# Optimization experiments

Hardware: AMD Instinct MI355X
Metric: run time of the kernel (lower is better)

Reference implementation:

```python
import jax, jax.numpy as jnp
import numpy as np

D_MODEL = 1024
HEADS = 16
DEPTH = D_MODEL // HEADS
B, S = 4, 4096
EPS_K = 1e-6  # kernel feature epsilon
EPS_LN = 1e-6


def setup_inputs() -> dict:
    key = jax.random.key(0)
    ks = jax.random.split(key, 8)
    lecun = 1.0 / np.sqrt(D_MODEL)  # LecunNormal stddev
    glorot = np.sqrt(2.0 / (D_MODEL + D_MODEL))  # keras Dense default
    return {
        "q": jax.random.normal(ks[0], (B, S, D_MODEL), jnp.float32),
        "k": jax.random.normal(ks[1], (B, S, D_MODEL), jnp.float32),
        "v": jax.random.normal(ks[2], (B, S, D_MODEL), jnp.float32),
        "mask": jnp.ones((B, S), jnp.float32),
        "wq": jax.random.normal(ks[3], (D_MODEL, D_MODEL), jnp.float32) * lecun,
        "wk": jax.random.normal(ks[4], (D_MODEL, D_MODEL), jnp.float32) * lecun,
        "wv": jax.random.normal(ks[5], (D_MODEL, D_MODEL), jnp.float32) * lecun,
        "ln_gamma": jnp.ones((D_MODEL,), jnp.float32),
        "ln_beta": jnp.zeros((D_MODEL,), jnp.float32),
        "dense_w": jax.random.normal(ks[6], (D_MODEL, D_MODEL), jnp.float32) * glorot,
        "dense_b": jnp.zeros((D_MODEL,), jnp.float32),
    }


def _layernorm(x, g, b):
    m = jnp.mean(x, axis=-1, keepdims=True)
    var = jnp.var(x, axis=-1, keepdims=True)
    return (x - m) * jax.lax.rsqrt(var + EPS_LN) * g + b


def _split_heads(x):
    bsz, sl, _ = x.shape
    return x.reshape(bsz, sl, HEADS, DEPTH).transpose(0, 2, 1, 3)  # [B,H,S,depth]


def reference(q, k, v, mask, wq, wk, wv, ln_gamma, ln_beta, dense_w, dense_b):
    bsz = q.shape[0]
    em = mask[:, None, :, None]  # [B,1,S,1] broadcast over heads/depth
    qh = _split_heads(_layernorm(q @ wq, ln_gamma, ln_beta))
    kh = _split_heads(_layernorm(k @ wk, ln_gamma, ln_beta))
    vh = _split_heads(_layernorm(v @ wv, ln_gamma, ln_beta))
    q_prime = jax.nn.relu(qh) + EPS_K
    k_prime = (jax.nn.relu(kh) + EPS_K) * em
    vh = vh * em
    kv = jnp.einsum('bhnd,bhne->bhde', k_prime, vh)  # [B,H,depth,depth]
    z = 1.0 / (jnp.einsum('bhnd,bhd->bhn', q_prime, k_prime.sum(axis=-2)) + EPS_K)
    att = jnp.einsum('bhnd,bhde,bhn->bhne', q_prime, kv, z)  # [B,H,S,depth]
    # Faithful to original: reshape WITHOUT transposing heads back.
    att = att.reshape(bsz, -1, D_MODEL)  # [B,S,d_model]
    out = att @ dense_w + dense_b
    return _layernorm(out, ln_gamma, ln_beta)
```

## Files before the change

### kernel.cpp

```cpp
#include <hip/hip_runtime.h>
#include <hip/hip_bf16.h>
#include <stdint.h>

#define D_MODEL 1024
#define S_LEN   4096
#define BATCH   4
#define HEADS   16
#define DEPTH   64
#define ROWS    (BATCH*S_LEN)
#define EPS_K_F 1e-6f
#define EPS_LN_F 1e-6f

typedef __attribute__((ext_vector_type(8))) short short8;
typedef __attribute__((ext_vector_type(4))) float f32x4;

__device__ __forceinline__ unsigned short f2bf(float f) {
  union { float f; unsigned u; } x; x.f = f;
  unsigned r = x.u + 0x7FFF + ((x.u >> 16) & 1);
  return (unsigned short)(r >> 16);
}
__device__ __forceinline__ float bf2f(unsigned short b) {
  union { unsigned u; float f; } x; x.u = ((unsigned)b) << 16;
  return x.f;
}
__device__ __forceinline__ void gload16(const void* g, void* l) {
  __builtin_amdgcn_global_load_lds(
      (const __attribute__((address_space(1))) void*)g,
      (__attribute__((address_space(3))) void*)l, 16, 0, 0);
}

__global__ __launch_bounds__(256) void wtrans_k(
    const float* __restrict__ W, unsigned short* __restrict__ Wt,
    const float* __restrict__ qsrc, unsigned short* __restrict__ qdst,
    int slice) {
  __shared__ float tile[32][33];
  int n0 = blockIdx.x * 32, k0 = blockIdx.y * 32;
  int tx = threadIdx.x & 31, ty = threadIdx.x >> 5;
  #pragma unroll
  for (int i = 0; i < 32; i += 8)
    tile[ty + i][tx] = W[(size_t)(k0 + ty + i) * D_MODEL + n0 + tx];
  if (qsrc) {
    int bid = blockIdx.y * 32 + blockIdx.x;
    size_t base = (size_t)slice * 4194304 + (size_t)bid * 4096 +
                  (size_t)threadIdx.x * 8;
    #pragma unroll
    for (int it = 0; it < 2; ++it) {
      size_t off = base + (size_t)it * 2048;
      float4 a = *(const float4*)(qsrc + off);
      float4 b = *(const float4*)(qsrc + off + 4);
      uint4 pk;
      pk.x = (unsigned)f2bf(a.x) | ((unsigned)f2bf(a.y) << 16);
      pk.y = (unsigned)f2bf(a.z) | ((unsigned)f2bf(a.w) << 16);
      pk.z = (unsigned)f2bf(b.x) | ((unsigned)f2bf(b.y) << 16);
      pk.w = (unsigned)f2bf(b.z) | ((unsigned)f2bf(b.w) << 16);
      *(uint4*)(qdst + off) = pk;
    }
  }
  __syncthreads();
  #pragma unroll
  for (int i = 0; i < 32; i += 8)
    Wt[(size_t)(n0 + ty + i) * D_MODEL + k0 + tx] = f2bf(tile[tx][ty + i]);
}


#define GEMM_EPILOGUE(HASBIAS)                                               \
  if (HASBIAS) {                                                             \
    float bv[4];                                                             \
    _Pragma("unroll")                                                        \
    for (int n = 0; n < 4; ++n)                                              \
      bv[n] = bias[(int)n0 + wcn * 64 + n * 16 + l15];                       \
    _Pragma("unroll")                                                        \
    for (int m = 0; m < 8; ++m)                                              \
      _Pragma("unroll")                                                      \
      for (int n = 0; n < 4; ++n)                                            \
        _Pragma("unroll")                                                    \
        for (int j = 0; j < 4; ++j)                                          \
          acc[m][n][j] += bv[n];                                             \
  }                                                                          \
  int seg = (int)(n0 >> 6) + wcn;                                            \
  _Pragma("unroll")                                                          \
  for (int m = 0; m < 8; ++m) {                                              \
    float s[4], s2[4];                                                       \
    _Pragma("unroll")                                                        \
    for (int j = 0; j < 4; ++j) {                                            \
      float a = 0.f, b = 0.f;                                                \
      _Pragma("unroll")                                                      \
      for (int n = 0; n < 4; ++n) { float x = acc[m][n][j]; a += x; b += x*x; } \
      s[j] = a; s2[j] = b;                                                   \
    }                                                                        \
    _Pragma("unroll")                                                        \
    for (int off = 1; off < 16; off <<= 1) {                                 \
      _Pragma("unroll")                                                      \
      for (int j = 0; j < 4; ++j) {                                          \
        s[j]  += __shfl_xor(s[j],  off);                                     \
        s2[j] += __shfl_xor(s2[j], off);                                     \
      }                                                                      \
    }                                                                        \
    if (l15 == 0) {                                                          \
      _Pragma("unroll")                                                      \
      for (int j = 0; j < 4; ++j) {                                          \
        int rg = (int)m0 + wr * 128 + m * 16 + lhi * 4 + j;                  \
        psum[rg * 16 + seg] = s[j];                                          \
        psq [rg * 16 + seg] = s2[j];                                         \
      }                                                                      \
    }                                                                        \
  }                                                                          \
  _Pragma("unroll")                                                          \
  for (int m = 0; m < 8; ++m)                                                \
    _Pragma("unroll")                                                        \
    for (int j = 0; j < 4; ++j) {                                            \
      size_t row = m0 + wr * 128 + m * 16 + lhi * 4 + j;                     \
      _Pragma("unroll")                                                      \
      for (int n = 0; n < 4; ++n) {                                          \
        int col = (int)n0 + wcn * 64 + n * 16 + l15;                         \
        Cb[row * N + col] = f2bf(acc[m][n][j]);                              \
      }                                                                      \
    }

#define STAGE_HALF(kof_, slot_, h_) do {                                     \
    _Pragma("unroll")                                                        \
    for (int j = 0; j < 2; ++j) {                                            \
      int idx = j * 512 + t; int r_ = idx >> 2; int cs_ = idx & 3;           \
      int c_ = cs_ ^ ((r_ >> 1) & 3);                                        \
      gload16(A + (m0 + r_) * (size_t)K + (kof_) + (h_) * 32 + c_ * 8,       \
              &Al[slot_][(h_) * 8192 + idx * 8]);                            \
    }                                                                        \
    _Pragma("unroll")                                                        \
    for (int j = 0; j < 2; ++j) {                                            \
      int idx = j * 512 + t; int r_ = idx >> 2; int cs_ = idx & 3;           \
      int c_ = cs_ ^ ((r_ >> 1) & 3);                                        \
      gload16(Bt + (n0 + r_) * (size_t)K + (kof_) + (h_) * 32 + c_ * 8,      \
              &Bl[slot_][(h_) * 8192 + idx * 8]);                            \
    }                                                                        \
  } while (0)

#define PH_READ_B(kk_)                                                       \
    _Pragma("unroll")                                                        \
    for (int n = 0; n < 4; ++n) {                                            \
      int rb_ = wcn * 64 + n * 16 + l15;                                     \
      bfr[n] = *(const short8*)&Bl[slot][(kk_) * 8192 + rb_ * 32 + cswz];    \
    }
#define PH_READ_A(kk_, mh_)                                                  \
    _Pragma("unroll")                                                        \
    for (int m = 0; m < 4; ++m) {                                            \
      int ra_ = wr * 128 + ((mh_) * 4 + m) * 16 + l15;                       \
      af[m] = *(const short8*)&Al[slot][(kk_) * 8192 + ra_ * 32 + cswz];     \
    }
#define PH_MFMA(mh_)                                                         \
    __builtin_amdgcn_s_setprio(1);                                           \
    _Pragma("unroll")                                                        \
    for (int m = 0; m < 4; ++m)                                              \
      _Pragma("unroll")                                                      \
      for (int n = 0; n < 4; ++n)                                            \
        acc[(mh_) * 4 + m][n] = __builtin_amdgcn_mfma_f32_16x16x32_bf16(     \
            af[m], bfr[n], acc[(mh_) * 4 + m][n], 0, 0, 0);                  \
    __builtin_amdgcn_s_setprio(0);
#define LGKM0                                                                \
    asm volatile("s_waitcnt lgkmcnt(0)" ::: "memory");                       \
    __builtin_amdgcn_sched_barrier(0);

#define SIDE_PACK_STORE(chunk_) do {                                         \
    uint4 pk_;                                                               \
    pk_.x = (unsigned)f2bf(sreg0.x) | ((unsigned)f2bf(sreg0.y) << 16);       \
    pk_.y = (unsigned)f2bf(sreg0.z) | ((unsigned)f2bf(sreg0.w) << 16);       \
    pk_.z = (unsigned)f2bf(sreg1.x) | ((unsigned)f2bf(sreg1.y) << 16);       \
    pk_.w = (unsigned)f2bf(sreg1.z) | ((unsigned)f2bf(sreg1.w) << 16);       \
    *(uint4*)(side_dst + sbase + (size_t)(chunk_) * 4096) = pk_;             \
  } while (0)
#define SIDE_LOAD(chunk_) do {                                               \
    const float* sp_ = side_src + sbase + (size_t)(chunk_) * 4096;           \
    sreg0 = *(const float4*)sp_; sreg1 = *(const float4*)(sp_ + 4);          \
  } while (0)

#define TAIL_TILE(slot_) do {                                                \
    const int slot = (slot_);                                                \
    short8 af[4], bfr[4];                                                    \
    PH_READ_B(0) PH_READ_A(0, 0) LGKM0 PH_MFMA(0)                            \
    PH_READ_A(0, 1) LGKM0 PH_MFMA(1)                                         \
    PH_READ_B(1) PH_READ_A(1, 0) LGKM0 PH_MFMA(0)                            \
    PH_READ_A(1, 1) LGKM0 PH_MFMA(1)                                         \
  } while (0)

template <bool SIDECAR>
__global__ __launch_bounds__(512) void gemm_bt_k(
    const unsigned short* __restrict__ A,
    const unsigned short* __restrict__ Bt,
    unsigned short* __restrict__ Cb,
    float* __restrict__ psum, float* __restrict__ psq,
    const float* __restrict__ bias,
    const float* __restrict__ side_src,
    unsigned short* __restrict__ side_dst,
    int M, int N, int K) {
  __shared__ unsigned short Al[2][16384];
  __shared__ unsigned short Bl[2][16384];
  int t = threadIdx.x;
  int lane = t & 63, wid = t >> 6;
  int wr = wid >> 2, wcn = wid & 3;
  int l15 = lane & 15, lhi = lane >> 4;
  const int cswz = (lhi ^ ((l15 >> 1) & 3)) << 3;
  int p = blockIdx.x;
  int cb = (p >> 3) & 3;
  int rb = (p & 7) | ((p >> 5) << 3);
  size_t m0 = (size_t)rb * 256, n0 = (size_t)cb * 256;
  f32x4 acc[8][4] = {};

  const int KT = K >> 6;

  float4 sreg0 = {}, sreg1 = {};
  size_t sbase = (size_t)p * 65536 + (size_t)t * 8;

  if (SIDECAR) SIDE_LOAD(0);
  STAGE_HALF(0, 0, 0);  STAGE_HALF(0, 0, 1);
  STAGE_HALF(64, 1, 0); STAGE_HALF(64, 1, 1);
  asm volatile("s_waitcnt vmcnt(8)" ::: "memory");
  __builtin_amdgcn_s_barrier();
  __builtin_amdgcn_sched_barrier(0);

  for (int kt = 0; kt < KT - 2; ++kt) {
    const int slot = kt & 1;
    short8 af[4], bfr[4];
    PH_READ_B(0)
    PH_READ_A(0, 0)
    LGKM0
    PH_MFMA(0)
    PH_READ_A(0, 1)
    LGKM0
    __builtin_amdgcn_s_barrier();
    __builtin_amdgcn_sched_barrier(0);
    STAGE_HALF((kt + 2) << 6, slot, 0);
    __builtin_amdgcn_sched_barrier(0);
    PH_MFMA(1)
    PH_READ_B(1)
    PH_READ_A(1, 0)
    LGKM0
    PH_MFMA(0)
    PH_READ_A(1, 1)
    LGKM0
    __builtin_amdgcn_s_barrier();
    __builtin_amdgcn_sched_barrier(0);
    STAGE_HALF((kt + 2) << 6, slot, 1);
    __builtin_amdgcn_sched_barrier(0);
    PH_MFMA(1)
    if (SIDECAR) {
      SIDE_PACK_STORE(kt);
      SIDE_LOAD(kt + 1);
      __builtin_amdgcn_sched_barrier(0);
      asm volatile("s_waitcnt vmcnt(11)" ::: "memory");
    } else {
      asm volatile("s_waitcnt vmcnt(8)" ::: "memory");
    }
    __builtin_amdgcn_s_barrier();
    __builtin_amdgcn_sched_barrier(0);
  }

  TAIL_TILE((KT - 2) & 1);
  if (SIDECAR) {
    SIDE_PACK_STORE(KT - 2);
    SIDE_LOAD(KT - 1);
    __builtin_amdgcn_sched_barrier(0);
    asm volatile("s_waitcnt vmcnt(3)" ::: "memory");
  } else {
    asm volatile("s_waitcnt vmcnt(0)" ::: "memory");
  }
  __builtin_amdgcn_s_barrier();
  __builtin_amdgcn_sched_barrier(0);

  TAIL_TILE((KT - 1) & 1);
  if (SIDECAR) SIDE_PACK_STORE(KT - 1);

  GEMM_EPILOGUE(bias != nullptr)
}

__global__ __launch_bounds__(256) void ln_stats_k(
    const float* __restrict__ psumK, const float* __restrict__ psqK,
    const float* __restrict__ psumV, const float* __restrict__ psqV,
    float* __restrict__ meanK, float* __restrict__ rstdK,
    float* __restrict__ meanV, float* __restrict__ rstdV) {
  int row = blockIdx.x * 256 + threadIdx.x;
  float sK = 0.f, s2K = 0.f, sV = 0.f, s2V = 0.f;
  #pragma unroll
  for (int i = 0; i < 16; ++i) {
    sK += psumK[row * 16 + i]; s2K += psqK[row * 16 + i];
    sV += psumV[row * 16 + i]; s2V += psqV[row * 16 + i];
  }
  float mK = sK * (1.f / D_MODEL);
  float mV = sV * (1.f / D_MODEL);
  meanK[row] = mK;
  rstdK[row] = rsqrtf(s2K * (1.f / D_MODEL) - mK * mK + EPS_LN_F);
  meanV[row] = mV;
  rstdV[row] = rsqrtf(s2V * (1.f / D_MODEL) - mV * mV + EPS_LN_F);
}

__global__ __launch_bounds__(256) void ln_act_k(
    const unsigned short* __restrict__ Cb,
    const float* __restrict__ psum, const float* __restrict__ psq,
    const float* __restrict__ gamma, const float* __restrict__ beta,
    unsigned short* __restrict__ out) {
  int row = blockIdx.x;
  int t = threadIdx.x;
  float s = 0.f, s2 = 0.f;
  #pragma unroll
  for (int i = 0; i < 16; ++i) { s += psum[row * 16 + i]; s2 += psq[row * 16 + i]; }
  float mean = s * (1.f / D_MODEL);
  float var = s2 * (1.f / D_MODEL) - mean * mean;
  float rstd = rsqrtf(var + EPS_LN_F);
  ushort4 cv = ((const ushort4*)(Cb + (size_t)row * D_MODEL))[t];
  float4 gv = ((const float4*)gamma)[t];
  float4 bv = ((const float4*)beta)[t];
  float av[4] = {bf2f(cv.x), bf2f(cv.y), bf2f(cv.z), bf2f(cv.w)};
  float g4[4] = {gv.x, gv.y, gv.z, gv.w};
  float b4[4] = {bv.x, bv.y, bv.z, bv.w};
  unsigned short ov[4];
  #pragma unroll
  for (int j = 0; j < 4; ++j) {
    float ln = (av[j] - mean) * rstd * g4[j] + b4[j];
    ov[j] = f2bf(fmaxf(ln, 0.f) + EPS_K_F);
  }
  ushort4 o; o.x = ov[0]; o.y = ov[1]; o.z = ov[2]; o.w = ov[3];
  ((ushort4*)(out + (size_t)row * D_MODEL))[t] = o;
}

__global__ __launch_bounds__(256) void ln_final_k(
    const unsigned short* __restrict__ Cb,
    const float* __restrict__ psum, const float* __restrict__ psq,
    const float* __restrict__ gamma, const float* __restrict__ beta,
    float* __restrict__ out) {
  int row = blockIdx.x;
  int t = threadIdx.x;
  float s = 0.f, s2 = 0.f;
  #pragma unroll
  for (int i = 0; i < 16; ++i) { s += psum[row * 16 + i]; s2 += psq[row * 16 + i]; }
  float mean = s * (1.f / D_MODEL);
  float var = s2 * (1.f / D_MODEL) - mean * mean;
  float rstd = rsqrtf(var + EPS_LN_F);
  ushort4 cv = ((const ushort4*)(Cb + (size_t)row * D_MODEL))[t];
  float4 gv = ((const float4*)gamma)[t];
  float4 bv = ((const float4*)beta)[t];
  float4 w;
  w.x = (bf2f(cv.x) - mean) * rstd * gv.x + bv.x;
  w.y = (bf2f(cv.y) - mean) * rstd * gv.y + bv.y;
  w.z = (bf2f(cv.z) - mean) * rstd * gv.z + bv.z;
  w.w = (bf2f(cv.w) - mean) * rstd * gv.w + bv.w;
  ((float4*)(out + (size_t)row * D_MODEL))[t] = w;
}

__global__ __launch_bounds__(256) void kv_mfma_k(
    const unsigned short* __restrict__ Ck, const unsigned short* __restrict__ Cv,
    const float* __restrict__ meanK, const float* __restrict__ rstdK,
    const float* __restrict__ meanV, const float* __restrict__ rstdV,
    const float* __restrict__ mask,
    const float* __restrict__ gamma, const float* __restrict__ beta,
    float* __restrict__ part, float* __restrict__ kspart) {
  __shared__ unsigned short Kl[4096];
  __shared__ unsigned short Vl[4096];
  int bh = blockIdx.y, chunk = blockIdx.x;
  int b_ = bh >> 4, h = bh & 15;
  int t = threadIdx.x, lane = t & 63, w = t >> 6;
  int l15 = lane & 15, g = lane >> 4;

  int sn = t >> 2, sd16 = t & 3;
  int sc = sd16 ^ ((sn >> 3) & 3);
  size_t goff = (size_t)sn * D_MODEL + h * DEPTH + sd16 * 16;
  int ldst = sn * 64 + sc * 16;

  float g16[16], b16[16];
  {
    int cbase = h * DEPTH + sd16 * 16;
    #pragma unroll
    for (int i = 0; i < 4; ++i) {
      float4 gv = *(const float4*)(gamma + cbase + i * 4);
      float4 bv = *(const float4*)(beta + cbase + i * 4);
      g16[i*4+0] = gv.x; g16[i*4+1] = gv.y; g16[i*4+2] = gv.z; g16[i*4+3] = gv.w;
      b16[i*4+0] = bv.x; b16[i*4+1] = bv.y; b16[i*4+2] = bv.z; b16[i*4+3] = bv.w;
    }
  }

  short8 ones;
  #pragma unroll
  for (int i = 0; i < 8; ++i) ones[i] = (short)0x3F80;

  f32x4 acc[4] = {};
  f32x4 ks = {};

  int baseA = ((w ^ g) << 4) + l15;
  int baseB0 = ((0 ^ g) << 4) + l15;
  int baseB1 = ((1 ^ g) << 4) + l15;
  int baseB2 = ((2 ^ g) << 4) + l15;
  int baseB3 = ((3 ^ g) << 4) + l15;

  int rowbase_r = b_ * S_LEN + chunk * 512;
  size_t rowbase = (size_t)rowbase_r * D_MODEL;
  for (int tile = 0; tile < 8; ++tile) {
    const unsigned short* kg = Ck + rowbase + (size_t)tile * 64 * D_MODEL + goff;
    const unsigned short* vg = Cv + rowbase + (size_t)tile * 64 * D_MODEL + goff;
    uint4 ra = *(const uint4*)kg;
    uint4 rb = *(const uint4*)(kg + 8);
    uint4 rc = *(const uint4*)vg;
    uint4 rd = *(const uint4*)(vg + 8);
    int grow = rowbase_r + tile * 64 + sn;
    float mk  = mask[grow];
    float mKv = meanK[grow], rKv = rstdK[grow];
    float mVv = meanV[grow], rVv = rstdV[grow];
    union { uint4 u[2]; unsigned short s[16]; } kin, vin, kout, vout;
    kin.u[0] = ra; kin.u[1] = rb;
    vin.u[0] = rc; vin.u[1] = rd;
    #pragma unroll
    for (int j = 0; j < 16; ++j) {
      float lnk = (bf2f(kin.s[j]) - mKv) * rKv * g16[j] + b16[j];
      kout.s[j] = f2bf((fmaxf(lnk, 0.f) + EPS_K_F) * mk);
      float lnv = (bf2f(vin.s[j]) - mVv) * rVv * g16[j] + b16[j];
      vout.s[j] = f2bf(lnv * mk);
    }
    __syncthreads();
    *(uint4*)&Kl[ldst]     = kout.u[0];
    *(uint4*)&Kl[ldst + 8] = kout.u[1];
    *(uint4*)&Vl[ldst]     = vout.u[0];
    *(uint4*)&Vl[ldst + 8] = vout.u[1];
    __syncthreads();
    #pragma unroll
    for (int kk = 0; kk < 2; ++kk) {
      int nb = (kk * 32 + g * 8) * 64;
      short8 af, bf0, bf1, bf2, bf3;
      #pragma unroll
      for (int i = 0; i < 8; ++i) {
        int rowoff = nb + i * 64;
        af[i]  = (short)Kl[rowoff + baseA];
        bf0[i] = (short)Vl[rowoff + baseB0];
        bf1[i] = (short)Vl[rowoff + baseB1];
        bf2[i] = (short)Vl[rowoff + baseB2];
        bf3[i] = (short)Vl[rowoff + baseB3];
      }
      acc[0] = __builtin_amdgcn_mfma_f32_16x16x32_bf16(af, bf0, acc[0], 0, 0, 0);
      acc[1] = __builtin_amdgcn_mfma_f32_16x16x32_bf16(af, bf1, acc[1], 0, 0, 0);
      acc[2] = __builtin_amdgcn_mfma_f32_16x16x32_bf16(af, bf2, acc[2], 0, 0, 0);
      acc[3] = __builtin_amdgcn_mfma_f32_16x16x32_bf16(af, bf3, acc[3], 0, 0, 0);
      ks     = __builtin_amdgcn_mfma_f32_16x16x32_bf16(af, ones, ks, 0, 0, 0);
    }
  }
  float* pp = part + ((size_t)bh * 8 + chunk) * 4096;
  #pragma unroll
  for (int nf = 0; nf < 4; ++nf)
    #pragma unroll
    for (int r = 0; r < 4; ++r)
      pp[(16 * w + 4 * g + r) * 64 + 16 * nf + l15] = acc[nf][r];
  if (l15 == 0) {
    #pragma unroll
    for (int r = 0; r < 4; ++r)
      kspart[((size_t)bh * 8 + chunk) * 64 + 16 * w + 4 * g + r] = ks[r];
  }
}

__global__ __launch_bounds__(256) void kv_reduce_k(
    const float* __restrict__ part, const float* __restrict__ kspart,
    unsigned short* __restrict__ KVT, float* __restrict__ ksum) {
  int bh = blockIdx.x, t = threadIdx.x;
  for (int idx = t; idx < 4096; idx += 256) {
    int d = idx >> 6, e = idx & 63;
    float s = 0.f;
    #pragma unroll
    for (int c = 0; c < 8; ++c)
      s += part[((size_t)bh * 8 + c) * 4096 + d * 64 + e];
    KVT[(size_t)bh * 4096 + e * 64 + d] = f2bf(s);
  }
  if (t < 64) {
    float s = 0.f;
    #pragma unroll
    for (int c = 0; c < 8; ++c) s += kspart[((size_t)bh * 8 + c) * 64 + t];
    ksum[bh * 64 + t] = s;
  }
}

__global__ __launch_bounds__(256) void att_k(
    const unsigned short* __restrict__ Qp, const unsigned short* __restrict__ KVT,
    const float* __restrict__ ksum, unsigned short* __restrict__ att) {
  __shared__ unsigned short Ql[128 * 64];
  __shared__ unsigned short Kl[64 * 64];
  __shared__ float ksl[64];
  __shared__ float zl[128];
  int bh = blockIdx.y;
  int b = bh >> 4, h = bh & 15;
  int r0 = blockIdx.x * 128;
  int t = threadIdx.x, lane = t & 63, wid = t >> 6;
  int l15 = lane & 15, lhi = lane >> 4;
  #pragma unroll
  for (int i = 0; i < 4; ++i) {
    int cid = i * 256 + t;
    int r = cid >> 3, c8 = cid & 7;
    gload16(Qp + ((size_t)(b * S_LEN + r0 + r)) * D_MODEL + h * DEPTH + c8 * 8,
            &Ql[cid * 8]);
  }
  #pragma unroll
  for (int i = 0; i < 2; ++i) {
    int cid = i * 256 + t;
    gload16(KVT + (size_t)bh * 4096 + cid * 8, &Kl[cid * 8]);
  }
  if (t < 64) ksl[t] = ksum[bh * 64 + t];
  asm volatile("s_waitcnt vmcnt(0)" ::: "memory");
  __syncthreads();
  {
    int r = t >> 1, half = t & 1;
    float s = 0.f;
    #pragma unroll
    for (int j = 0; j < 32; ++j)
      s += bf2f(Ql[r * 64 + half * 32 + j]) * ksl[half * 32 + j];
    s += __shfl_xor(s, 1);
    if (half == 0) zl[r] = 1.f / (s + EPS_K_F);
  }
  __syncthreads();
  f32x4 acc[2][4] = {};
  #pragma unroll
  for (int kk = 0; kk < 2; ++kk) {
    short8 af[2], bfr[4];
    #pragma unroll
    for (int m = 0; m < 2; ++m)
      af[m] = *(const short8*)&Ql[(wid * 32 + m * 16 + l15) * 64 + kk * 32 + lhi * 8];
    #pragma unroll
    for (int n = 0; n < 4; ++n)
      bfr[n] = *(const short8*)&Kl[(n * 16 + l15) * 64 + kk * 32 + lhi * 8];
    #pragma unroll
    for (int m = 0; m < 2; ++m)
      #pragma unroll
      for (int n = 0; n < 4; ++n)
        acc[m][n] = __builtin_amdgcn_mfma_f32_16x16x32_bf16(af[m], bfr[n], acc[m][n], 0, 0, 0);
  }
  #pragma unroll
  for (int m = 0; m < 2; ++m)
    #pragma unroll
    for (int j = 0; j < 4; ++j) {
      int rl = wid * 32 + m * 16 + lhi * 4 + j;
      int n = r0 + rl;
      float z = zl[rl];
      #pragma unroll
      for (int nf = 0; nf < 4; ++nf) {
        int ee = nf * 16 + l15;
        size_t orow = (size_t)b * S_LEN + h * 256 + (n >> 4);
        int ocol = (n & 15) * 64 + ee;
        att[orow * D_MODEL + ocol] = f2bf(acc[m][nf][j] * z);
      }
    }
}

extern "C" void kernel_launch(void* const* d_in, const int* in_sizes, int n_in,
                              void* d_out, int out_size, void* d_ws, size_t ws_size,
                              hipStream_t stream) {
  (void)in_sizes; (void)n_in; (void)out_size; (void)ws_size;
  const float* q     = (const float*)d_in[0];
  const float* k     = (const float*)d_in[1];
  const float* v     = (const float*)d_in[2];
  const float* mask  = (const float*)d_in[3];
  const float* wq    = (const float*)d_in[4];
  const float* wk    = (const float*)d_in[5];
  const float* wv    = (const float*)d_in[6];
  const float* gamma = (const float*)d_in[7];
  const float* beta  = (const float*)d_in[8];
  const float* dw    = (const float*)d_in[9];
  const float* db    = (const float*)d_in[10];
  float* out = (float*)d_out;

  char* ws = (char*)d_ws;
  unsigned short* Xq  = (unsigned short*)(ws);
  unsigned short* Xk  = (unsigned short*)(ws + 33554432);
  unsigned short* Xv  = (unsigned short*)(ws + 67108864);
  unsigned short* Qp  = Xq;
  unsigned short* Cd  = Xq;
  unsigned short* WqT = (unsigned short*)(ws + 100663296);
  unsigned short* WkT = WqT + 1048576;
  unsigned short* WvT = WkT + 1048576;
  unsigned short* WdT = WvT + 1048576;
  float* part   = (float*)(ws + 109051904);
  float* kspart = (float*)(ws + 117440512);
  unsigned short* KVT = (unsigned short*)(ws + 117964800);
  float* ksum = (float*)(ws + 118489088);
  float* psum  = (float*)(ws + 119537664);
  float* psq   = (float*)(ws + 120586240);
  float* psumK = (float*)(ws + 121634816);
  float* psqK  = (float*)(ws + 122683392);
  float* psumV = (float*)(ws + 123731968);
  float* psqV  = (float*)(ws + 124780544);
  float* meanK = (float*)(ws + 125829120);
  float* rstdK = (float*)(ws + 125894656);
  float* meanV = (float*)(ws + 125960192);
  float* rstdV = (float*)(ws + 126025728);
  unsigned short* Cq = (unsigned short*)d_out;
  unsigned short* Ck = (unsigned short*)d_out;
  unsigned short* Cv = (unsigned short*)((char*)d_out + 33554432);
  unsigned short* Catt = (unsigned short*)d_out;

  dim3 b256(256);
  dim3 b512(512);
  dim3 wtg(32, 32);
  dim3 gemmg(256);
  dim3 lng(ROWS);

  wtrans_k<<<wtg, b256, 0, stream>>>(wq, WqT, q, Xq, 0);
  wtrans_k<<<wtg, b256, 0, stream>>>(wk, WkT, q, Xq, 1);
  wtrans_k<<<wtg, b256, 0, stream>>>(wv, WvT, q, Xq, 2);
  wtrans_k<<<wtg, b256, 0, stream>>>(dw, WdT, q, Xq, 3);

  gemm_bt_k<true><<<gemmg, b512, 0, stream>>>(Xq, WqT, Cq, psum, psq, nullptr,
                                              k, Xk, ROWS, D_MODEL, D_MODEL);
  ln_act_k<<<lng, b256, 0, stream>>>(Cq, psum, psq, gamma, beta, Qp);

  gemm_bt_k<true><<<gemmg, b512, 0, stream>>>(Xk, WkT, Ck, psumK, psqK, nullptr,
                                              v, Xv, ROWS, D_MODEL, D_MODEL);
  gemm_bt_k<false><<<gemmg, b512, 0, stream>>>(Xv, WvT, Cv, psumV, psqV, nullptr,
                                               nullptr, nullptr, ROWS, D_MODEL, D_MODEL);

  ln_stats_k<<<dim3(64), b256, 0, stream>>>(psumK, psqK, psumV, psqV,
                                            meanK, rstdK, meanV, rstdV);

  kv_mfma_k<<<dim3(8, 64), b256, 0, stream>>>(Ck, Cv, meanK, rstdK, meanV, rstdV,
                                              mask, gamma, beta, part, kspart);
  kv_reduce_k<<<dim3(64), b256, 0, stream>>>(part, kspart, KVT, ksum);
  att_k<<<dim3(32, 64), b256, 0, stream>>>(Qp, KVT, ksum, Catt);

  gemm_bt_k<false><<<gemmg, b512, 0, stream>>>(Catt, WdT, Cd, psum, psq, db,
                                               nullptr, nullptr, ROWS, D_MODEL, D_MODEL);
  ln_final_k<<<lng, b256, 0, stream>>>(Cd, psum, psq, gamma, beta, out);
}
```

Before: 310.9 us.

## Fuse Q layernorm+ReLU into attention kernel and merge weight transposes

Removes the separate ln_act_k pass over the Q projection. Q row stats are now computed in ln_stats_k, and att_k applies the layernorm, ReLU and epsilon while staging Q into LDS through an XOR-swizzled layout. The four weight-transpose launches are merged into one 3D-grid launch. Workspace buffers are remapped so Ck, Catt and Cd live in the workspace while Cq stays in the output buffer. This saves one full read and write of a 32 MB bf16 tensor plus launch overhead, at the cost of more per-block ALU work and register pressure in att_k.

Result: faster. 293.1 us (-5.7%).

```diff
diff --git a/kernel.cpp b/kernel.cpp
--- a/kernel.cpp
+++ b/kernel.cpp
@@ -29,20 +29,24 @@
       (__attribute__((address_space(3))) void*)l, 16, 0, 0);
 }
 
-__global__ __launch_bounds__(256) void wtrans_k(
-    const float* __restrict__ W, unsigned short* __restrict__ Wt,
-    const float* __restrict__ qsrc, unsigned short* __restrict__ qdst,
-    int slice) {
+__global__ __launch_bounds__(256) void wtrans4_k(
+    const float* __restrict__ w0, const float* __restrict__ w1,
+    const float* __restrict__ w2, const float* __restrict__ w3,
+    unsigned short* __restrict__ t0, unsigned short* __restrict__ t1,
+    unsigned short* __restrict__ t2, unsigned short* __restrict__ t3,
+    const float* __restrict__ qsrc, unsigned short* __restrict__ qdst) {
   __shared__ float tile[32][33];
+  int z = blockIdx.z;
+  const float* W = (z == 0) ? w0 : (z == 1) ? w1 : (z == 2) ? w2 : w3;
+  unsigned short* Wt = (z == 0) ? t0 : (z == 1) ? t1 : (z == 2) ? t2 : t3;
   int n0 = blockIdx.x * 32, k0 = blockIdx.y * 32;
   int tx = threadIdx.x & 31, ty = threadIdx.x >> 5;
   #pragma unroll
   for (int i = 0; i < 32; i += 8)
     tile[ty + i][tx] = W[(size_t)(k0 + ty + i) * D_MODEL + n0 + tx];
-  if (qsrc) {
-    int bid = blockIdx.y * 32 + blockIdx.x;
-    size_t base = (size_t)slice * 4194304 + (size_t)bid * 4096 +
-                  (size_t)threadIdx.x * 8;
+  {
+    int bid = (z * 32 + blockIdx.y) * 32 + blockIdx.x;
+    size_t base = (size_t)bid * 4096 + (size_t)threadIdx.x * 8;
     #pragma unroll
     for (int it = 0; it < 2; ++it) {
       size_t off = base + (size_t)it * 2048;
@@ -272,52 +276,29 @@
 }
 
 __global__ __launch_bounds__(256) void ln_stats_k(
+    const float* __restrict__ psumQ, const float* __restrict__ psqQ,
     const float* __restrict__ psumK, const float* __restrict__ psqK,
     const float* __restrict__ psumV, const float* __restrict__ psqV,
+    float* __restrict__ meanQ, float* __restrict__ rstdQ,
     float* __restrict__ meanK, float* __restrict__ rstdK,
     float* __restrict__ meanV, float* __restrict__ rstdV) {
   int row = blockIdx.x * 256 + threadIdx.x;
-  float sK = 0.f, s2K = 0.f, sV = 0.f, s2V = 0.f;
+  float sQ = 0.f, s2Q = 0.f, sK = 0.f, s2K = 0.f, sV = 0.f, s2V = 0.f;
   #pragma unroll
   for (int i = 0; i < 16; ++i) {
+    sQ += psumQ[row * 16 + i]; s2Q += psqQ[row * 16 + i];
     sK += psumK[row * 16 + i]; s2K += psqK[row * 16 + i];
     sV += psumV[row * 16 + i]; s2V += psqV[row * 16 + i];
   }
+  float mQ = sQ * (1.f / D_MODEL);
   float mK = sK * (1.f / D_MODEL);
   float mV = sV * (1.f / D_MODEL);
+  meanQ[row] = mQ;
+  rstdQ[row] = rsqrtf(s2Q * (1.f / D_MODEL) - mQ * mQ + EPS_LN_F);
   meanK[row] = mK;
   rstdK[row] = rsqrtf(s2K * (1.f / D_MODEL) - mK * mK + EPS_LN_F);
   meanV[row] = mV;
   rstdV[row] = rsqrtf(s2V * (1.f / D_MODEL) - mV * mV + EPS_LN_F);
-}
-
-__global__ __launch_bounds__(256) void ln_act_k(
-    const unsigned short* __restrict__ Cb,
-    const float* __restrict__ psum, const float* __restrict__ psq,
-    const float* __restrict__ gamma, const float* __restrict__ beta,
-    unsigned short* __restrict__ out) {
-  int row = blockIdx.x;
-  int t = threadIdx.x;
-  float s = 0.f, s2 = 0.f;
-  #pragma unroll
-  for (int i = 0; i < 16; ++i) { s += psum[row * 16 + i]; s2 += psq[row * 16 + i]; }
-  float mean = s * (1.f / D_MODEL);
-  float var = s2 * (1.f / D_MODEL) - mean * mean;
-  float rstd = rsqrtf(var + EPS_LN_F);
-  ushort4 cv = ((const ushort4*)(Cb + (size_t)row * D_MODEL))[t];
-  float4 gv = ((const float4*)gamma)[t];
-  float4 bv = ((const float4*)beta)[t];
-  float av[4] = {bf2f(cv.x), bf2f(cv.y), bf2f(cv.z), bf2f(cv.w)};
-  float g4[4] = {gv.x, gv.y, gv.z, gv.w};
-  float b4[4] = {bv.x, bv.y, bv.z, bv.w};
-  unsigned short ov[4];
-  #pragma unroll
-  for (int j = 0; j < 4; ++j) {
-    float ln = (av[j] - mean) * rstd * g4[j] + b4[j];
-    ov[j] = f2bf(fmaxf(ln, 0.f) + EPS_K_F);
-  }
-  ushort4 o; o.x = ov[0]; o.y = ov[1]; o.z = ov[2]; o.w = ov[3];
-  ((ushort4*)(out + (size_t)row * D_MODEL))[t] = o;
 }
 
 __global__ __launch_bounds__(256) void ln_final_k(
@@ -471,7 +452,10 @@
 }
 
 __global__ __launch_bounds__(256) void att_k(
-    const unsigned short* __restrict__ Qp, const unsigned short* __restrict__ KVT,
+    const unsigned short* __restrict__ Cq,
+    const float* __restrict__ meanQ, const float* __restrict__ rstdQ,
+    const float* __restrict__ gamma, const float* __restrict__ beta,
+    const unsigned short* __restrict__ KVT,
     const float* __restrict__ ksum, unsigned short* __restrict__ att) {
   __shared__ unsigned short Ql[128 * 64];
   __shared__ unsigned short Kl[64 * 64];
@@ -482,27 +466,52 @@
   int r0 = blockIdx.x * 128;
   int t = threadIdx.x, lane = t & 63, wid = t >> 6;
   int l15 = lane & 15, lhi = lane >> 4;
-  #pragma unroll
-  for (int i = 0; i < 4; ++i) {
-    int cid = i * 256 + t;
-    int r = cid >> 3, c8 = cid & 7;
-    gload16(Qp + ((size_t)(b * S_LEN + r0 + r)) * D_MODEL + h * DEPTH + c8 * 8,
-            &Ql[cid * 8]);
-  }
+
   #pragma unroll
   for (int i = 0; i < 2; ++i) {
     int cid = i * 256 + t;
     gload16(KVT + (size_t)bh * 4096 + cid * 8, &Kl[cid * 8]);
   }
   if (t < 64) ksl[t] = ksum[bh * 64 + t];
+
+  {
+    int r = t & 127, half = t >> 7;
+    int grow = b * S_LEN + r0 + r;
+    float mean = meanQ[grow], rstd = rstdQ[grow];
+    int cbase = h * DEPTH + half * 32;
+    float g32[32], b32[32];
+    #pragma unroll
+    for (int i = 0; i < 8; ++i) {
+      float4 gv = *(const float4*)(gamma + cbase + i * 4);
+      float4 bv = *(const float4*)(beta + cbase + i * 4);
+      g32[i*4+0] = gv.x; g32[i*4+1] = gv.y; g32[i*4+2] = gv.z; g32[i*4+3] = gv.w;
+      b32[i*4+0] = bv.x; b32[i*4+1] = bv.y; b32[i*4+2] = bv.z; b32[i*4+3] = bv.w;
+    }
+    const unsigned short* src = Cq + (size_t)grow * D_MODEL + cbase;
+    #pragma unroll
+    for (int i = 0; i < 4; ++i) {
+      union { uint4 u; unsigned short s[8]; } in, outp;
+      in.u = *(const uint4*)(src + i * 8);
+      #pragma unroll
+      for (int j = 0; j < 8; ++j) {
+        float ln = (bf2f(in.s[j]) - mean) * rstd * g32[i*8+j] + b32[i*8+j];
+        outp.s[j] = f2bf(fmaxf(ln, 0.f) + EPS_K_F);
+      }
+      int cg = half * 4 + i;
+      *(uint4*)&Ql[r * 64 + ((cg ^ (r & 7)) << 3)] = outp.u;
+    }
+  }
   asm volatile("s_waitcnt vmcnt(0)" ::: "memory");
   __syncthreads();
   {
     int r = t >> 1, half = t & 1;
     float s = 0.f;
     #pragma unroll
-    for (int j = 0; j < 32; ++j)
-      s += bf2f(Ql[r * 64 + half * 32 + j]) * ksl[half * 32 + j];
+    for (int j = 0; j < 32; ++j) {
+      int col = half * 32 + j;
+      s += bf2f(Ql[r * 64 + (((col >> 3) ^ (r & 7)) << 3) + (col & 7)]) *
+           ksl[col];
+    }
     s += __shfl_xor(s, 1);
     if (half == 0) zl[r] = 1.f / (s + EPS_K_F);
   }
@@ -512,8 +521,11 @@
   for (int kk = 0; kk < 2; ++kk) {
     short8 af[2], bfr[4];
     #pragma unroll
-    for (int m = 0; m < 2; ++m)
-      af[m] = *(const short8*)&Ql[(wid * 32 + m * 16 + l15) * 64 + kk * 32 + lhi * 8];
+    for (int m = 0; m < 2; ++m) {
+      int rr = wid * 32 + m * 16 + l15;
+      int cx = kk * 4 + lhi;
+      af[m] = *(const short8*)&Ql[rr * 64 + ((cx ^ (rr & 7)) << 3)];
+    }
     #pragma unroll
     for (int n = 0; n < 4; ++n)
       bfr[n] = *(const short8*)&Kl[(n * 16 + l15) * 64 + kk * 32 + lhi * 8];
@@ -559,10 +571,11 @@
 
   char* ws = (char*)d_ws;
   unsigned short* Xq  = (unsigned short*)(ws);
+  unsigned short* Ck  = (unsigned short*)(ws);
+  unsigned short* Cd  = (unsigned short*)(ws);
   unsigned short* Xk  = (unsigned short*)(ws + 33554432);
+  unsigned short* Catt= (unsigned short*)(ws + 33554432);
   unsigned short* Xv  = (unsigned short*)(ws + 67108864);
-  unsigned short* Qp  = Xq;
-  unsigned short* Cd  = Xq;
   unsigned short* WqT = (unsigned short*)(ws + 100663296);
   unsigned short* WkT = WqT + 1048576;
   unsigned short* WvT = WkT + 1048576;
@@ -570,49 +583,47 @@
   float* part   = (float*)(ws + 109051904);
   float* kspart = (float*)(ws + 117440512);
   unsigned short* KVT = (unsigned short*)(ws + 117964800);
-  float* ksum = (float*)(ws + 118489088);
+  float* ksum  = (float*)(ws + 118489088);
   float* psum  = (float*)(ws + 119537664);
   float* psq   = (float*)(ws + 120586240);
   float* psumK = (float*)(ws + 121634816);
   float* psqK  = (float*)(ws + 122683392);
   float* psumV = (float*)(ws + 123731968);
   float* psqV  = (float*)(ws + 124780544);
-  float* meanK = (float*)(ws + 125829120);
-  float* rstdK = (float*)(ws + 125894656);
-  float* meanV = (float*)(ws + 125960192);
-  float* rstdV = (float*)(ws + 126025728);
+  float* psumQ = (float*)(ws + 125829120);
+  float* psqQ  = (float*)(ws + 126877696);
+  float* meanK = (float*)(ws + 127926272);
+  float* rstdK = (float*)(ws + 127991808);
+  float* meanV = (float*)(ws + 128057344);
+  float* rstdV = (float*)(ws + 128122880);
+  float* meanQ = (float*)(ws + 128188416);
+  float* rstdQ = (float*)(ws + 128253952);
   unsigned short* Cq = (unsigned short*)d_out;
-  unsigned short* Ck = (unsigned short*)d_out;
   unsigned short* Cv = (unsigned short*)((char*)d_out + 33554432);
-  unsigned short* Catt = (unsigned short*)d_out;
 
   dim3 b256(256);
   dim3 b512(512);
-  dim3 wtg(32, 32);
+  dim3 wtg(32, 32, 4);
   dim3 gemmg(256);
   dim3 lng(ROWS);
 
-  wtrans_k<<<wtg, b256, 0, stream>>>(wq, WqT, q, Xq, 0);
-  wtrans_k<<<wtg, b256, 0, stream>>>(wk, WkT, q, Xq, 1);
-  wtrans_k<<<wtg, b256, 0, stream>>>(wv, WvT, q, Xq, 2);
-  wtrans_k<<<wtg, b256, 0, stream>>>(dw, WdT, q, Xq, 3);
-
-  gemm_bt_k<true><<<gemmg, b512, 0, stream>>>(Xq, WqT, Cq, psum, psq, nullptr,
+  wtrans4_k<<<wtg, b256, 0, stream>>>(wq, wk, wv, dw, WqT, WkT, WvT, WdT, q, Xq);
+
+  gemm_bt_k<true><<<gemmg, b512, 0, stream>>>(Xq, WqT, Cq, psumQ, psqQ, nullptr,
                                               k, Xk, ROWS, D_MODEL, D_MODEL);
-  ln_act_k<<<lng, b256, 0, stream>>>(Cq, psum, psq, gamma, beta, Qp);
-
   gemm_bt_k<true><<<gemmg, b512, 0, stream>>>(Xk, WkT, Ck, psumK, psqK, nullptr,
                                               v, Xv, ROWS, D_MODEL, D_MODEL);
   gemm_bt_k<false><<<gemmg, b512, 0, stream>>>(Xv, WvT, Cv, psumV, psqV, nullptr,
                                                nullptr, nullptr, ROWS, D_MODEL, D_MODEL);
 
-  ln_stats_k<<<dim3(64), b256, 0, stream>>>(psumK, psqK, psumV, psqV,
-                                            meanK, rstdK, meanV, rstdV);
+  ln_stats_k<<<dim3(64), b256, 0, stream>>>(psumQ, psqQ, psumK, psqK, psumV, psqV,
+                                            meanQ, rstdQ, meanK, rstdK, meanV, rstdV);
 
   kv_mfma_k<<<dim3(8, 64), b256, 0, stream>>>(Ck, Cv, meanK, rstdK, meanV, rstdV,
                                               mask, gamma, beta, part, kspart);
   kv_reduce_k<<<dim3(64), b256, 0, stream>>>(part, kspart, KVT, ksum);
-  att_k<<<dim3(32, 64), b256, 0, stream>>>(Qp, KVT, ksum, Catt);
+  att_k<<<dim3(32, 64), b256, 0, stream>>>(Cq, meanQ, rstdQ, gamma, beta,
+                                           KVT, ksum, Catt);
 
   gemm_bt_k<false><<<gemmg, b512, 0, stream>>>(Catt, WdT, Cd, psum, psq, db,
                                                nullptr, nullptr, ROWS, D_MODEL, D_MODEL);
```
